# Optimization experiments

Hardware: AMD Instinct MI355X
Metric: run time of the kernel (lower is better)

## Reference

```python
import jax, jax.numpy as jnp
import numpy as np

B, C_LEN, Q_LEN, DIM = 8, 2048, 512, 512


def setup_inputs() -> dict:
    key = jax.random.key(0)
    ks = jax.random.split(key, 6)
    s = 1.0 / np.sqrt(DIM).astype(np.float32)
    return {
        "C": jax.random.normal(ks[0], (C_LEN, B, DIM), jnp.float32),
        "Q": jax.random.normal(ks[1], (Q_LEN, B, DIM), jnp.float32),
        "C_mask": jnp.ones((C_LEN, B), jnp.int32),
        "Q_mask": jnp.ones((Q_LEN, B), jnp.int32),
        "Wq": jax.random.normal(ks[2], (DIM, DIM), jnp.float32) * s,
        "bq": jnp.zeros((DIM,), jnp.float32),
        "w1": jax.random.normal(ks[3], (DIM,), jnp.float32) * s,
        "w2": jax.random.normal(ks[4], (DIM,), jnp.float32) * s,
        "w3": jax.random.normal(ks[5], (DIM,), jnp.float32) * s,
        "b": jnp.zeros((), jnp.float32),
    }


def reference(C, Q, C_mask, Q_mask, Wq, bq, w1, w2, w3, b):
    # seq-first -> batch-first
    Cb = jnp.transpose(C, (1, 0, 2))   # [B, c_len, d]
    Qb = jnp.transpose(Q, (1, 0, 2))   # [B, q_len, d]
    Cm = C_mask.T                      # [B, c_len]
    Qm = Q_mask.T                      # [B, q_len]

    Qp = Qb @ Wq + bq                  # Q_linear: [B, q_len, d]

    # Trilinear score S[b,i,j] = w1.C_i + w2.Q_j + w3.(C_i*Q_j) + b
    # (decomposed form of Linear(cat(C, Q, C*Q)) -> avoids [B,c,q,3d] blowup)
    S = ((Cb @ w1)[:, :, None]
         + (Qp @ w2)[:, None, :]
         + jnp.einsum('bid,bjd->bij', Cb * w3, Qp)
         + b)                          # [B, c_len, q_len]

    neg_inf = jnp.float32(-jnp.inf)
    S_row = jax.nn.softmax(jnp.where(Qm[:, None, :] == 0, neg_inf, S), axis=2)
    S_col = jax.nn.softmax(jnp.where(Cm[:, :, None] == 0, neg_inf, S), axis=1)

    A = S_row @ Qp                                        # [B, c_len, d]
    # (S_row @ S_col^T) @ C == S_row @ (S_col^T @ C), cheaper association
    Bm = S_row @ jnp.einsum('bij,bid->bjd', S_col, Cb)    # [B, c_len, d]

    CQ = jnp.concatenate((Cb, A, Cb * A, Cb * Bm), axis=-1)  # [B, c_len, 4d]
    return jnp.transpose(CQ, (1, 0, 2))                      # [c_len, B, 4d]
```

## Files before the change

kernel.cpp:

```cpp
#include <hip/hip_runtime.h>
#include <math.h>

constexpr int BB = 8;
constexpr int CL = 2048;
constexpr int QL = 512;
constexpr int DM = 512;

typedef short          bf16x8 __attribute__((ext_vector_type(8)));
typedef unsigned short us8    __attribute__((ext_vector_type(8)));
typedef float          f32x4  __attribute__((ext_vector_type(4)));

__device__ __forceinline__ unsigned short f2b(float f) {
  union { float f; unsigned u; } v; v.f = f;
  return (unsigned short)((v.u + 0x7FFFu + ((v.u >> 16) & 1u)) >> 16);
}

enum { G_QP = 0, G_S = 1, G_SLOT = 2, G_TT = 3 };

template <int MODE, int WR, int WC>
__global__ __launch_bounds__(WR * WC * 64) void mgemm(
    const unsigned short* __restrict__ A, int sA, size_t batA,
    const unsigned short* __restrict__ B, int sB, size_t batB,
    int K,
    float* __restrict__ Of, unsigned short* __restrict__ Ob,
    int sD, size_t batD,
    const float* __restrict__ e1, const float* __restrict__ e2,
    const float* __restrict__ e3)
{
  const int tid = threadIdx.x, b = blockIdx.z;
  const int wave = tid >> 6, lane = tid & 63;
  const int wr = wave / WC, wc = wave % WC;
  const int m0 = blockIdx.x * (WR * 64) + wr * 64;
  const int n0 = blockIdx.y * (WC * 64) + wc * 64;
  const int l15 = lane & 15, lk8 = (lane >> 4) * 8;

  const unsigned short* ap = A + batA * b + (size_t)(m0 + l15) * sA + lk8;
  const unsigned short* bp = B + batB * b + (size_t)(n0 + l15) * sB + lk8;

  f32x4 acc[4][4];
  #pragma unroll
  for (int mr = 0; mr < 4; mr++)
    #pragma unroll
    for (int nc = 0; nc < 4; nc++) acc[mr][nc] = (f32x4){0.f, 0.f, 0.f, 0.f};

  for (int k0 = 0; k0 < K; k0 += 32) {
    bf16x8 af[4], bf[4];
    #pragma unroll
    for (int mr = 0; mr < 4; mr++)
      af[mr] = *(const bf16x8*)(ap + (size_t)mr * 16 * sA + k0);
    #pragma unroll
    for (int nc = 0; nc < 4; nc++)
      bf[nc] = *(const bf16x8*)(bp + (size_t)nc * 16 * sB + k0);
    #pragma unroll
    for (int mr = 0; mr < 4; mr++)
      #pragma unroll
      for (int nc = 0; nc < 4; nc++)
        acc[mr][nc] = __builtin_amdgcn_mfma_f32_16x16x32_bf16(
            af[mr], bf[nc], acc[mr][nc], 0, 0, 0);
  }

  const int r0 = (lane >> 4) * 4;
  #pragma unroll
  for (int mr = 0; mr < 4; mr++) {
    #pragma unroll
    for (int nc = 0; nc < 4; nc++) {
      const int col = n0 + nc * 16 + l15;
      float addc = 0.f;
      if constexpr (MODE == G_QP) addc = e1[col];
      if constexpr (MODE == G_S)  addc = e2[b * QL + col] + e3[0];
      #pragma unroll
      for (int r = 0; r < 4; r++) {
        const int row = m0 + mr * 16 + r0 + r;
        float v = acc[mr][nc][r] + addc;
        if constexpr (MODE == G_S) v += e1[b * CL + row];
        if constexpr (MODE == G_TT)
          Ob[batD * b + (size_t)row * sD + col] = f2b(v);
        else
          Of[batD * b + (size_t)row * sD + col] = v;
      }
    }
  }
}

__global__ __launch_bounds__(256) void cast8(const float* __restrict__ src,
                                             unsigned short* __restrict__ dst)
{
  const int g = blockIdx.x * 256 + threadIdx.x;
  const float4 v0 = *((const float4*)src + g * 2);
  const float4 v1 = *((const float4*)src + g * 2 + 1);
  us8 r = {f2b(v0.x), f2b(v0.y), f2b(v0.z), f2b(v0.w),
           f2b(v1.x), f2b(v1.y), f2b(v1.z), f2b(v1.w)};
  *((us8*)dst + g) = r;
}

__global__ __launch_bounds__(256) void build_cw3(const float* __restrict__ C,
                                                 const float* __restrict__ w3,
                                                 unsigned short* __restrict__ dst)
{
  const int g = blockIdx.x * 256 + threadIdx.x;
  const int orow = g >> 6, d0 = (g & 63) * 8;
  const int b = orow >> 11, i = orow & 2047;
  const float* s = C + ((size_t)i * BB + b) * DM + d0;
  const float4 v0 = *(const float4*)s, v1 = *(const float4*)(s + 4);
  const float4 w0 = *(const float4*)(w3 + d0), w1 = *(const float4*)(w3 + d0 + 4);
  us8 r = {f2b(v0.x * w0.x), f2b(v0.y * w0.y), f2b(v0.z * w0.z), f2b(v0.w * w0.w),
           f2b(v1.x * w1.x), f2b(v1.y * w1.y), f2b(v1.z * w1.z), f2b(v1.w * w1.w)};
  *(us8*)(dst + (size_t)orow * DM + d0) = r;
}

__global__ __launch_bounds__(256) void transbf(const float* __restrict__ src,
                                               unsigned short* __restrict__ dst,
                                               int sSrc, int sDst,
                                               size_t batSrc, size_t batDst)
{
  __shared__ float t[64][65];
  const int b = blockIdx.z;
  const int r0 = blockIdx.x * 64, c0 = blockIdx.y * 64;
  const int tx = threadIdx.x & 63, ty = threadIdx.x >> 6;
  const float* S = src + batSrc * b;
  unsigned short* D = dst + batDst * b;
  #pragma unroll
  for (int rr = 0; rr < 16; rr++) {
    const int r = ty * 16 + rr;
    t[r][tx] = S[(size_t)(r0 + r) * sSrc + c0 + tx];
  }
  __syncthreads();
  #pragma unroll
  for (int rr = 0; rr < 16; rr++) {
    const int c = ty * 16 + rr;
    D[(size_t)(c0 + c) * sDst + r0 + tx] = f2b(t[tx][c]);
  }
}

__global__ __launch_bounds__(256) void build_prow(
    const float* __restrict__ S, const int* __restrict__ qm,
    const float* __restrict__ rmax, const float* __restrict__ rinv,
    unsigned short* __restrict__ dst)
{
  const int g = blockIdx.x * 256 + threadIdx.x;
  const int row = g >> 6, j0 = (g & 63) * 8;
  const int b = row >> 11;
  const float* s = S + (size_t)row * QL + j0;
  const float4 v0 = *(const float4*)s, v1 = *(const float4*)(s + 4);
  const float m = rmax[row], iv = rinv[row];
  const float va[8] = {v0.x, v0.y, v0.z, v0.w, v1.x, v1.y, v1.z, v1.w};
  us8 r;
  #pragma unroll
  for (int e = 0; e < 8; e++) {
    const int mk = qm[(j0 + e) * BB + b];
    r[e] = mk ? f2b(expf(va[e] - m) * iv) : (unsigned short)0;
  }
  *(us8*)(dst + (size_t)row * QL + j0) = r;
}

__global__ __launch_bounds__(256) void build_pcolt(
    const float* __restrict__ Sm, const int* __restrict__ cm,
    const float* __restrict__ cmax, const float* __restrict__ cinv,
    unsigned short* __restrict__ dst)
{
  __shared__ float t[64][65];
  const int b = blockIdx.z;
  const int i0 = blockIdx.x * 64, j0 = blockIdx.y * 64;
  const int tx = threadIdx.x & 63, ty = threadIdx.x >> 6;
  const float* S = Sm + (size_t)b * CL * QL;
  #pragma unroll
  for (int rr = 0; rr < 16; rr++) {
    const int i = ty * 16 + rr;
    t[i][tx] = S[(size_t)(i0 + i) * QL + j0 + tx];
  }
  __syncthreads();
  const int cmv = cm[(i0 + tx) * BB + b];
  #pragma unroll
  for (int rr = 0; rr < 16; rr++) {
    const int j = j0 + ty * 16 + rr;
    const float mj = cmax[b * QL + j], ivj = cinv[b * QL + j];
    const float v = t[tx][ty * 16 + rr];
    dst[(size_t)b * QL * CL + (size_t)j * CL + i0 + tx] =
        cmv ? f2b(expf(v - mj) * ivj) : (unsigned short)0;
  }
}

template <int MAP>
__global__ __launch_bounds__(256) void rowdot(const float* __restrict__ src,
                                              const float* __restrict__ w,
                                              float* __restrict__ out)
{
  const int rid = blockIdx.x * 4 + (threadIdx.x >> 6);
  const int lane = threadIdx.x & 63;
  const float* row;
  if constexpr (MAP == 1) {
    const int b = rid >> 11, i = rid & 2047;
    row = src + ((size_t)i * BB + b) * DM;
  } else {
    row = src + (size_t)rid * DM;
  }
  float4 v0 = *(const float4*)(row + lane * 8);
  float4 v1 = *(const float4*)(row + lane * 8 + 4);
  float4 w0 = *(const float4*)(w + lane * 8);
  float4 w1 = *(const float4*)(w + lane * 8 + 4);
  float s = v0.x * w0.x + v0.y * w0.y + v0.z * w0.z + v0.w * w0.w +
            v1.x * w1.x + v1.y * w1.y + v1.z * w1.z + v1.w * w1.w;
  #pragma unroll
  for (int off = 32; off; off >>= 1) s += __shfl_xor(s, off);
  if (lane == 0) out[rid] = s;
}

__global__ __launch_bounds__(256) void row_stats(const float* __restrict__ S,
    const int* __restrict__ qm, float* __restrict__ rmax, float* __restrict__ rinv)
{
  const int rid = blockIdx.x * 4 + (threadIdx.x >> 6);
  const int lane = threadIdx.x & 63;
  const int b = rid >> 11;
  const float* row = S + (size_t)rid * QL;
  float4 v0 = *(const float4*)(row + lane * 8);
  float4 v1 = *(const float4*)(row + lane * 8 + 4);
  float va[8] = {v0.x, v0.y, v0.z, v0.w, v1.x, v1.y, v1.z, v1.w};
  int mk[8];
  float m = -INFINITY;
  #pragma unroll
  for (int e = 0; e < 8; e++) {
    mk[e] = qm[(lane * 8 + e) * BB + b];
    if (mk[e]) m = fmaxf(m, va[e]);
  }
  #pragma unroll
  for (int off = 32; off; off >>= 1) m = fmaxf(m, __shfl_xor(m, off));
  float s = 0.f;
  #pragma unroll
  for (int e = 0; e < 8; e++) if (mk[e]) s += expf(va[e] - m);
  #pragma unroll
  for (int off = 32; off; off >>= 1) s += __shfl_xor(s, off);
  if (lane == 0) { rmax[rid] = m; rinv[rid] = 1.f / s; }
}

constexpr int CH = 16;

__global__ __launch_bounds__(256) void col_part(const float* __restrict__ S,
    const int* __restrict__ cm, float* __restrict__ pmax, float* __restrict__ psum)
{
  const int t = blockIdx.x * 256 + threadIdx.x;
  const int ch = blockIdx.y;
  const int b = t >> 9, j = t & 511;
  const float* col = S + (size_t)b * CL * QL + j;
  float m = -INFINITY, s = 0.f;
  const int i0 = ch * (CL / CH);
  for (int i = 0; i < CL / CH; i++) {
    const int ig = i0 + i;
    const float v = col[(size_t)ig * QL];
    if (cm[ig * BB + b]) {
      const float nm = fmaxf(m, v);
      s = s * expf(m - nm) + expf(v - nm);
      m = nm;
    }
  }
  pmax[ch * 4096 + t] = m;
  psum[ch * 4096 + t] = s;
}

__global__ __launch_bounds__(256) void col_comb(const float* __restrict__ pmax,
    const float* __restrict__ psum, float* __restrict__ cmax, float* __restrict__ cinv)
{
  const int t = blockIdx.x * 256 + threadIdx.x;
  float m = -INFINITY;
  #pragma unroll
  for (int ch = 0; ch < CH; ch++) m = fmaxf(m, pmax[ch * 4096 + t]);
  float s = 0.f;
  #pragma unroll
  for (int ch = 0; ch < CH; ch++) {
    const float pm = pmax[ch * 4096 + t];
    if (pm > -INFINITY) s += psum[ch * 4096 + t] * expf(pm - m);
  }
  cmax[t] = m;
  cinv[t] = 1.f / s;
}

__global__ __launch_bounds__(256) void assemble(const float* __restrict__ Cin,
                                                float* __restrict__ out)
{
  const size_t f = (size_t)blockIdx.x * 256 + threadIdx.x;
  const size_t row = f >> 7, d4 = f & 127;
  const float4 c = ((const float4*)Cin)[row * 128 + d4];
  float4* orow = (float4*)out + row * 512;
  const float4 a = orow[128 + d4];
  const float4 bm = orow[384 + d4];
  orow[d4] = c;
  float4 ca = {c.x * a.x, c.y * a.y, c.z * a.z, c.w * a.w};
  float4 cb = {c.x * bm.x, c.y * bm.y, c.z * bm.z, c.w * bm.w};
  orow[256 + d4] = ca;
  orow[384 + d4] = cb;
}

extern "C" void kernel_launch(void* const* d_in, const int* in_sizes, int n_in,
                              void* d_out, int out_size, void* d_ws, size_t ws_size,
                              hipStream_t stream)
{
  const float* C  = (const float*)d_in[0];
  const float* Q  = (const float*)d_in[1];
  const int*   Cm = (const int*)d_in[2];
  const int*   Qm = (const int*)d_in[3];
  const float* Wq = (const float*)d_in[4];
  const float* bq = (const float*)d_in[5];
  const float* w1 = (const float*)d_in[6];
  const float* w2 = (const float*)d_in[7];
  const float* w3 = (const float*)d_in[8];
  const float* bs = (const float*)d_in[9];
  float* out = (float*)d_out;
  float* ws  = (float*)d_ws;

  float* S    = ws;
  float* Qp   = ws + 8388608;
  float* c1   = ws + 10485760;
  float* q2   = ws + 10502144;
  float* rmax = ws + 10506240;
  float* rinv = ws + 10522624;
  float* cmax = ws + 10539008;
  float* cinv = ws + 10543104;
  float* pmax = ws + 10547200;
  float* psum = ws + 10612736;
  unsigned short* bfp   = (unsigned short*)(ws + 10678272);
  unsigned short* Qb    = bfp;
  unsigned short* Qpb   = bfp;
  unsigned short* Ttb   = bfp;
  unsigned short* Wqt   = bfp + 2097152;
  unsigned short* Cw3b  = bfp + 2359296;
  unsigned short* Prow  = bfp + 2359296;
  unsigned short* Qpbt  = bfp + 10747904;
  unsigned short* PcolT = bfp + 12845056;
  unsigned short* Cbt   = (unsigned short*)S;

  cast8<<<1024, 256, 0, stream>>>(Q, Qb);
  transbf<<<dim3(8, 8, 1), 256, 0, stream>>>(Wq, Wqt, DM, DM, 0, 0);
  build_cw3<<<4096, 256, 0, stream>>>(C, w3, Cw3b);
  rowdot<1><<<4096, 256, 0, stream>>>(C, w1, c1);

  mgemm<G_QP, 1, 2><<<dim3(8, 4, BB), 128, 0, stream>>>(
      Qb, BB * DM, DM, Wqt, DM, 0, DM,
      Qp, nullptr, DM, (size_t)QL * DM, bq, nullptr, nullptr);
  cast8<<<1024, 256, 0, stream>>>(Qp, Qpb);
  transbf<<<dim3(8, 8, BB), 256, 0, stream>>>(Qp, Qpbt, DM, QL,
                                              (size_t)QL * DM, (size_t)DM * QL);
  rowdot<0><<<1024, 256, 0, stream>>>(Qp, w2, q2);

  mgemm<G_S, 2, 2><<<dim3(16, 4, BB), 256, 0, stream>>>(
      Cw3b, DM, (size_t)CL * DM, Qpb, DM, (size_t)QL * DM, DM,
      S, nullptr, QL, (size_t)CL * QL, c1, q2, bs);

  row_stats<<<4096, 256, 0, stream>>>(S, Qm, rmax, rinv);
  col_part<<<dim3(16, CH), 256, 0, stream>>>(S, Cm, pmax, psum);
  col_comb<<<16, 256, 0, stream>>>(pmax, psum, cmax, cinv);

  build_prow<<<4096, 256, 0, stream>>>(S, Qm, rmax, rinv, Prow);
  build_pcolt<<<dim3(32, 8, BB), 256, 0, stream>>>(S, Cm, cmax, cinv, PcolT);

  transbf<<<dim3(32, 8, BB), 256, 0, stream>>>(C, Cbt, BB * DM, CL,
                                               DM, (size_t)DM * CL);

  mgemm<G_TT, 1, 2><<<dim3(8, 4, BB), 128, 0, stream>>>(
      Cbt, CL, (size_t)DM * CL, PcolT, CL, (size_t)QL * CL, CL,
      nullptr, Ttb, QL, (size_t)DM * QL, nullptr, nullptr, nullptr);

  mgemm<G_SLOT, 2, 2><<<dim3(16, 4, BB), 256, 0, stream>>>(
      Prow, QL, (size_t)CL * QL, Qpbt, QL, (size_t)DM * QL, QL,
      out + 512, nullptr, BB * 4 * DM, (size_t)4 * DM, nullptr, nullptr, nullptr);

  mgemm<G_SLOT, 2, 2><<<dim3(16, 4, BB), 256, 0, stream>>>(
      Prow, QL, (size_t)CL * QL, Ttb, QL, (size_t)DM * QL, QL,
      out + 1536, nullptr, BB * 4 * DM, (size_t)4 * DM, nullptr, nullptr, nullptr);

  assemble<<<8192, 256, 0, stream>>>(C, out);
}
```

Baseline: 504.0 us.

## Fuse elementwise passes into GEMM epilogues and merge softmax row kernels

Several small kernels are folded into neighbours. The w1 row-dot moves into the C*w3 cast kernel. The Qp bf16 cast moves into the Q-projection GEMM epilogue. Row stats and row probability construction become one row_softmax kernel. The final assemble pass is replaced by GEMM epilogues that write C, A, C*A and C*Bm straight into the output. This removes launches and the extra global-memory round trips through S and the output buffer, at the cost of uncoalesced, strided epilogue writes and extra C reads inside the GEMMs.

```diff
diff --git a/kernel.cpp b/kernel.cpp
--- a/kernel.cpp
+++ b/kernel.cpp
@@ -15,7 +15,7 @@
   return (unsigned short)((v.u + 0x7FFFu + ((v.u >> 16) & 1u)) >> 16);
 }
 
-enum { G_QP = 0, G_S = 1, G_SLOT = 2, G_TT = 3 };
+enum { G_QP = 0, G_S = 1, G_TT = 2, G_A = 3, G_BM = 4 };
 
 template <int MODE, int WR, int WC>
 __global__ __launch_bounds__(WR * WC * 64) void mgemm(
@@ -66,17 +66,31 @@
     for (int nc = 0; nc < 4; nc++) {
       const int col = n0 + nc * 16 + l15;
       float addc = 0.f;
-      if constexpr (MODE == G_QP) addc = e1[col];
+      if constexpr (MODE == G_QP) addc = e2[col];
       if constexpr (MODE == G_S)  addc = e2[b * QL + col] + e3[0];
       #pragma unroll
       for (int r = 0; r < 4; r++) {
         const int row = m0 + mr * 16 + r0 + r;
         float v = acc[mr][nc][r] + addc;
-        if constexpr (MODE == G_S) v += e1[b * CL + row];
-        if constexpr (MODE == G_TT)
+        if constexpr (MODE == G_S) {
+          v += e1[b * CL + row];
+          Of[batD * b + (size_t)row * sD + col] = v;
+        } else if constexpr (MODE == G_QP) {
+          Of[batD * b + (size_t)row * sD + col] = v;
           Ob[batD * b + (size_t)row * sD + col] = f2b(v);
-        else
-          Of[batD * b + (size_t)row * sD + col] = v;
+        } else if constexpr (MODE == G_TT) {
+          Ob[batD * b + (size_t)row * sD + col] = f2b(v);
+        } else {
+          const size_t obase = ((size_t)row * BB + b) * (4 * DM) + col;
+          const float c = e1[((size_t)row * BB + b) * DM + col];
+          if constexpr (MODE == G_A) {
+            Of[obase] = c;
+            Of[obase + DM] = v;
+            Of[obase + 2 * DM] = c * v;
+          } else {
+            Of[obase + 3 * DM] = c * v;
+          }
+        }
       }
     }
   }
@@ -93,19 +107,26 @@
   *((us8*)dst + g) = r;
 }
 
-__global__ __launch_bounds__(256) void build_cw3(const float* __restrict__ C,
-                                                 const float* __restrict__ w3,
-                                                 unsigned short* __restrict__ dst)
+__global__ __launch_bounds__(256) void build_cw3c(
+    const float* __restrict__ C, const float* __restrict__ w3,
+    const float* __restrict__ w1, unsigned short* __restrict__ dst,
+    float* __restrict__ c1)
 {
   const int g = blockIdx.x * 256 + threadIdx.x;
   const int orow = g >> 6, d0 = (g & 63) * 8;
   const int b = orow >> 11, i = orow & 2047;
   const float* s = C + ((size_t)i * BB + b) * DM + d0;
   const float4 v0 = *(const float4*)s, v1 = *(const float4*)(s + 4);
-  const float4 w0 = *(const float4*)(w3 + d0), w1 = *(const float4*)(w3 + d0 + 4);
-  us8 r = {f2b(v0.x * w0.x), f2b(v0.y * w0.y), f2b(v0.z * w0.z), f2b(v0.w * w0.w),
-           f2b(v1.x * w1.x), f2b(v1.y * w1.y), f2b(v1.z * w1.z), f2b(v1.w * w1.w)};
+  const float4 w30 = *(const float4*)(w3 + d0), w31 = *(const float4*)(w3 + d0 + 4);
+  const float4 w10 = *(const float4*)(w1 + d0), w11 = *(const float4*)(w1 + d0 + 4);
+  us8 r = {f2b(v0.x * w30.x), f2b(v0.y * w30.y), f2b(v0.z * w30.z), f2b(v0.w * w30.w),
+           f2b(v1.x * w31.x), f2b(v1.y * w31.y), f2b(v1.z * w31.z), f2b(v1.w * w31.w)};
   *(us8*)(dst + (size_t)orow * DM + d0) = r;
+  float sdot = v0.x * w10.x + v0.y * w10.y + v0.z * w10.z + v0.w * w10.w +
+               v1.x * w11.x + v1.y * w11.y + v1.z * w11.z + v1.w * w11.w;
+  #pragma unroll
+  for (int off = 32; off; off >>= 1) sdot += __shfl_xor(sdot, off);
+  if ((g & 63) == 0) c1[orow] = sdot;
 }
 
 __global__ __launch_bounds__(256) void transbf(const float* __restrict__ src,
@@ -132,25 +153,37 @@
   }
 }
 
-__global__ __launch_bounds__(256) void build_prow(
+__global__ __launch_bounds__(256) void row_softmax(
     const float* __restrict__ S, const int* __restrict__ qm,
-    const float* __restrict__ rmax, const float* __restrict__ rinv,
     unsigned short* __restrict__ dst)
 {
-  const int g = blockIdx.x * 256 + threadIdx.x;
-  const int row = g >> 6, j0 = (g & 63) * 8;
-  const int b = row >> 11;
-  const float* s = S + (size_t)row * QL + j0;
-  const float4 v0 = *(const float4*)s, v1 = *(const float4*)(s + 4);
-  const float m = rmax[row], iv = rinv[row];
+  const int rid = blockIdx.x * 4 + (threadIdx.x >> 6);
+  const int lane = threadIdx.x & 63;
+  const int b = rid >> 11;
+  const float* row = S + (size_t)rid * QL;
+  const float4 v0 = *(const float4*)(row + lane * 8);
+  const float4 v1 = *(const float4*)(row + lane * 8 + 4);
   const float va[8] = {v0.x, v0.y, v0.z, v0.w, v1.x, v1.y, v1.z, v1.w};
+  int mk[8];
+  float m = -INFINITY;
+  #pragma unroll
+  for (int e = 0; e < 8; e++) {
+    mk[e] = qm[(lane * 8 + e) * BB + b];
+    if (mk[e]) m = fmaxf(m, va[e]);
+  }
+  #pragma unroll
+  for (int off = 32; off; off >>= 1) m = fmaxf(m, __shfl_xor(m, off));
+  float s = 0.f;
+  #pragma unroll
+  for (int e = 0; e < 8; e++) if (mk[e]) s += expf(va[e] - m);
+  #pragma unroll
+  for (int off = 32; off; off >>= 1) s += __shfl_xor(s, off);
+  const float iv = 1.f / s;
   us8 r;
   #pragma unroll
-  for (int e = 0; e < 8; e++) {
-    const int mk = qm[(j0 + e) * BB + b];
-    r[e] = mk ? f2b(expf(va[e] - m) * iv) : (unsigned short)0;
-  }
-  *(us8*)(dst + (size_t)row * QL + j0) = r;
+  for (int e = 0; e < 8; e++)
+    r[e] = mk[e] ? f2b(expf(va[e] - m) * iv) : (unsigned short)0;
+  *(us8*)(dst + (size_t)rid * QL + lane * 8) = r;
 }
 
 __global__ __launch_bounds__(256) void build_pcolt(
@@ -180,20 +213,13 @@
   }
 }
 
-template <int MAP>
 __global__ __launch_bounds__(256) void rowdot(const float* __restrict__ src,
                                               const float* __restrict__ w,
                                               float* __restrict__ out)
 {
   const int rid = blockIdx.x * 4 + (threadIdx.x >> 6);
   const int lane = threadIdx.x & 63;
-  const float* row;
-  if constexpr (MAP == 1) {
-    const int b = rid >> 11, i = rid & 2047;
-    row = src + ((size_t)i * BB + b) * DM;
-  } else {
-    row = src + (size_t)rid * DM;
-  }
+  const float* row = src + (size_t)rid * DM;
   float4 v0 = *(const float4*)(row + lane * 8);
   float4 v1 = *(const float4*)(row + lane * 8 + 4);
   float4 w0 = *(const float4*)(w + lane * 8);
@@ -203,33 +229,6 @@
   #pragma unroll
   for (int off = 32; off; off >>= 1) s += __shfl_xor(s, off);
   if (lane == 0) out[rid] = s;
-}
-
-__global__ __launch_bounds__(256) void row_stats(const float* __restrict__ S,
-    const int* __restrict__ qm, float* __restrict__ rmax, float* __restrict__ rinv)
-{
-  const int rid = blockIdx.x * 4 + (threadIdx.x >> 6);
-  const int lane = threadIdx.x & 63;
-  const int b = rid >> 11;
-  const float* row = S + (size_t)rid * QL;
-  float4 v0 = *(const float4*)(row + lane * 8);
-  float4 v1 = *(const float4*)(row + lane * 8 + 4);
-  float va[8] = {v0.x, v0.y, v0.z, v0.w, v1.x, v1.y, v1.z, v1.w};
-  int mk[8];
-  float m = -INFINITY;
-  #pragma unroll
-  for (int e = 0; e < 8; e++) {
-    mk[e] = qm[(lane * 8 + e) * BB + b];
-    if (mk[e]) m = fmaxf(m, va[e]);
-  }
-  #pragma unroll
-  for (int off = 32; off; off >>= 1) m = fmaxf(m, __shfl_xor(m, off));
-  float s = 0.f;
-  #pragma unroll
-  for (int e = 0; e < 8; e++) if (mk[e]) s += expf(va[e] - m);
-  #pragma unroll
-  for (int off = 32; off; off >>= 1) s += __shfl_xor(s, off);
-  if (lane == 0) { rmax[rid] = m; rinv[rid] = 1.f / s; }
 }
 
 constexpr int CH = 16;
@@ -273,22 +272,6 @@
   cinv[t] = 1.f / s;
 }
 
-__global__ __launch_bounds__(256) void assemble(const float* __restrict__ Cin,
-                                                float* __restrict__ out)
-{
-  const size_t f = (size_t)blockIdx.x * 256 + threadIdx.x;
-  const size_t row = f >> 7, d4 = f & 127;
-  const float4 c = ((const float4*)Cin)[row * 128 + d4];
-  float4* orow = (float4*)out + row * 512;
-  const float4 a = orow[128 + d4];
-  const float4 bm = orow[384 + d4];
-  orow[d4] = c;
-  float4 ca = {c.x * a.x, c.y * a.y, c.z * a.z, c.w * a.w};
-  float4 cb = {c.x * bm.x, c.y * bm.y, c.z * bm.z, c.w * bm.w};
-  orow[256 + d4] = ca;
-  orow[384 + d4] = cb;
-}
-
 extern "C" void kernel_launch(void* const* d_in, const int* in_sizes, int n_in,
                               void* d_out, int out_size, void* d_ws, size_t ws_size,
                               hipStream_t stream)
@@ -310,45 +293,40 @@
   float* Qp   = ws + 8388608;
   float* c1   = ws + 10485760;
   float* q2   = ws + 10502144;
-  float* rmax = ws + 10506240;
-  float* rinv = ws + 10522624;
-  float* cmax = ws + 10539008;
-  float* cinv = ws + 10543104;
-  float* pmax = ws + 10547200;
-  float* psum = ws + 10612736;
-  unsigned short* bfp   = (unsigned short*)(ws + 10678272);
+  float* cmax = ws + 10506240;
+  float* cinv = ws + 10510336;
+  float* pmax = ws + 10514432;
+  float* psum = ws + 10579968;
+  unsigned short* bfp   = (unsigned short*)(ws + 10645504);
   unsigned short* Qb    = bfp;
-  unsigned short* Qpb   = bfp;
   unsigned short* Ttb   = bfp;
   unsigned short* Wqt   = bfp + 2097152;
   unsigned short* Cw3b  = bfp + 2359296;
   unsigned short* Prow  = bfp + 2359296;
-  unsigned short* Qpbt  = bfp + 10747904;
-  unsigned short* PcolT = bfp + 12845056;
+  unsigned short* Qpb   = bfp + 10747904;
+  unsigned short* Qpbt  = bfp + 12845056;
+  unsigned short* PcolT = bfp + 14942208;
   unsigned short* Cbt   = (unsigned short*)S;
 
   cast8<<<1024, 256, 0, stream>>>(Q, Qb);
   transbf<<<dim3(8, 8, 1), 256, 0, stream>>>(Wq, Wqt, DM, DM, 0, 0);
-  build_cw3<<<4096, 256, 0, stream>>>(C, w3, Cw3b);
-  rowdot<1><<<4096, 256, 0, stream>>>(C, w1, c1);
+  build_cw3c<<<4096, 256, 0, stream>>>(C, w3, w1, Cw3b, c1);
 
   mgemm<G_QP, 1, 2><<<dim3(8, 4, BB), 128, 0, stream>>>(
       Qb, BB * DM, DM, Wqt, DM, 0, DM,
-      Qp, nullptr, DM, (size_t)QL * DM, bq, nullptr, nullptr);
-  cast8<<<1024, 256, 0, stream>>>(Qp, Qpb);
+      Qp, Qpb, DM, (size_t)QL * DM, nullptr, bq, nullptr);
   transbf<<<dim3(8, 8, BB), 256, 0, stream>>>(Qp, Qpbt, DM, QL,
                                               (size_t)QL * DM, (size_t)DM * QL);
-  rowdot<0><<<1024, 256, 0, stream>>>(Qp, w2, q2);
+  rowdot<<<1024, 256, 0, stream>>>(Qp, w2, q2);
 
   mgemm<G_S, 2, 2><<<dim3(16, 4, BB), 256, 0, stream>>>(
       Cw3b, DM, (size_t)CL * DM, Qpb, DM, (size_t)QL * DM, DM,
       S, nullptr, QL, (size_t)CL * QL, c1, q2, bs);
 
-  row_stats<<<4096, 256, 0, stream>>>(S, Qm, rmax, rinv);
+  row_softmax<<<4096, 256, 0, stream>>>(S, Qm, Prow);
+
   col_part<<<dim3(16, CH), 256, 0, stream>>>(S, Cm, pmax, psum);
   col_comb<<<16, 256, 0, stream>>>(pmax, psum, cmax, cinv);
-
-  build_prow<<<4096, 256, 0, stream>>>(S, Qm, rmax, rinv, Prow);
   build_pcolt<<<dim3(32, 8, BB), 256, 0, stream>>>(S, Cm, cmax, cinv, PcolT);
 
   transbf<<<dim3(32, 8, BB), 256, 0, stream>>>(C, Cbt, BB * DM, CL,
@@ -358,13 +336,11 @@
       Cbt, CL, (size_t)DM * CL, PcolT, CL, (size_t)QL * CL, CL,
       nullptr, Ttb, QL, (size_t)DM * QL, nullptr, nullptr, nullptr);
 
-  mgemm<G_SLOT, 2, 2><<<dim3(16, 4, BB), 256, 0, stream>>>(
+  mgemm<G_A, 2, 2><<<dim3(16, 4, BB), 256, 0, stream>>>(
       Prow, QL, (size_t)CL * QL, Qpbt, QL, (size_t)DM * QL, QL,
-      out + 512, nullptr, BB * 4 * DM, (size_t)4 * DM, nullptr, nullptr, nullptr);
-
-  mgemm<G_SLOT, 2, 2><<<dim3(16, 4, BB), 256, 0, stream>>>(
+      out, nullptr, 0, 0, C, nullptr, nullptr);
+
+  mgemm<G_BM, 2, 2><<<dim3(16, 4, BB), 256, 0, stream>>>(
       Prow, QL, (size_t)CL * QL, Ttb, QL, (size_t)DM * QL, QL,
-      out + 1536, nullptr, BB * 4 * DM, (size_t)4 * DM, nullptr, nullptr, nullptr);
-
-  assemble<<<8192, 256, 0, stream>>>(C, out);
-}
+      out, nullptr, 0, 0, C, nullptr, nullptr);
+}
```

After: 478.0 us. 5.2% less time.
